# Kernel tuning notes

Hardware: AMD Instinct MI355X
Metric: run time of the kernel (lower is better)

## Reference

```python
import jax, jax.numpy as jnp
import numpy as np

FUSION_RATIO = 0.1


def graph_conv(src, dst, x, W, b, n):
    # DGL GraphConv, norm='both': h = D_in^{-1/2} A D_out^{-1/2} (x W) + b
    ones = jnp.ones((src.shape[0],), x.dtype)
    deg_out = jnp.clip(jax.ops.segment_sum(ones, src, num_segments=n), 1.0)
    deg_in = jnp.clip(jax.ops.segment_sum(ones, dst, num_segments=n), 1.0)
    h = (x @ W) * (deg_out ** -0.5)[:, None]
    agg = jax.ops.segment_sum(h[src], dst, num_segments=n)  # [n, out]
    return agg * (deg_in ** -0.5)[:, None] + b


def norm_embed(e):
    # z-score (unbiased std, matching torch.std) then min-max
    e = (e - e.mean()) / jnp.std(e, ddof=1)
    return (e - e.min()) / (e.max() - e.min())


def setup_inputs() -> dict:
    key = jax.random.key(0)
    ks = jax.random.split(key, 24)
    n_apig, n_fcg = 50000, 100000
    e_apig, e_fcg = 800000, 1600000
    apig_dim, fcg_dim, hidden, united, ncls = 256, 128, 128, 64, 10
    s = 0.05
    inp = {
        'apig_feat': jax.random.normal(ks[0], (n_apig, apig_dim), jnp.float32),
        'fcg_feat': jax.random.normal(ks[1], (n_fcg, fcg_dim), jnp.float32),
        'W_a1': jax.random.normal(ks[2], (apig_dim, hidden), jnp.float32) * s,
        'b_a1': jnp.zeros((hidden,), jnp.float32),
        'W_a2': jax.random.normal(ks[3], (hidden, hidden), jnp.float32) * s,
        'b_a2': jnp.zeros((hidden,), jnp.float32),
        'W_f1': jax.random.normal(ks[4], (fcg_dim, hidden), jnp.float32) * s,
        'b_f1': jnp.zeros((hidden,), jnp.float32),
        'W_f2': jax.random.normal(ks[5], (hidden, hidden), jnp.float32) * s,
        'b_f2': jnp.zeros((hidden,), jnp.float32),
        'W1': jax.random.normal(ks[6], (hidden, united), jnp.float32) * s,
        'b1': jnp.zeros((united,), jnp.float32),
        'W2': jax.random.normal(ks[7], (united, hidden), jnp.float32) * s,
        'b2': jnp.zeros((hidden,), jnp.float32),
        'W_attn': jax.random.normal(ks[8], (hidden, 1), jnp.float32) * s,
        'b_attn': jnp.zeros((1,), jnp.float32),
        'W_cls': jax.random.normal(ks[9], (hidden, ncls), jnp.float32) * s,
        'b_cls': jnp.zeros((ncls,), jnp.float32),
        'apig_src': jax.random.randint(ks[10], (e_apig,), 0, n_apig, jnp.int32),
        'apig_dst': jax.random.randint(ks[11], (e_apig,), 0, n_apig, jnp.int32),
        'fcg_src': jax.random.randint(ks[12], (e_fcg,), 0, n_fcg, jnp.int32),
        'fcg_dst': jax.random.randint(ks[13], (e_fcg,), 0, n_fcg, jnp.int32),
        'n_apig': n_apig,
        'n_fcg': n_fcg,
    }
    return inp


def reference(apig_feat, fcg_feat, W_a1, b_a1, W_a2, b_a2, W_f1, b_f1, W_f2, b_f2,
              W1, b1, W2, b2, W_attn, b_attn, W_cls, b_cls,
              apig_src, apig_dst, fcg_src, fcg_dst, n_apig, n_fcg):
    h_a1 = jax.nn.relu(graph_conv(apig_src, apig_dst, apig_feat, W_a1, b_a1, n_apig))
    h_f1 = jax.nn.relu(graph_conv(fcg_src, fcg_dst, fcg_feat, W_f1, b_f1, n_fcg))
    a_enc = h_a1 @ W1 + b1
    f_enc = h_f1 @ W1 + b1
    a_sum = a_enc.sum(axis=0)
    f_sum = f_enc.sum(axis=0)
    a_enc = a_enc + FUSION_RATIO * f_sum
    f_enc = f_enc + FUSION_RATIO * a_sum
    a_dec = a_enc @ W2 + b2
    f_dec = f_enc @ W2 + b2
    h_a2 = jax.nn.relu(graph_conv(apig_src, apig_dst, a_dec, W_a2, b_a2, n_apig))
    h_f2 = jax.nn.relu(graph_conv(fcg_src, fcg_dst, f_dec, W_f2, b_f2, n_fcg))
    apig_emb = h_a2.mean(axis=0)  # dgl.mean_nodes, single graph -> [hidden]
    fcg_emb = h_f2.max(axis=0)    # dgl.max_nodes -> [hidden]
    a = norm_embed(apig_emb)
    f = norm_embed(fcg_emb)
    wa = jax.nn.softmax(a @ W_attn + b_attn, axis=0)  # [1] -> 1.0
    wf = jax.nn.softmax(f @ W_attn + b_attn, axis=0)
    emb = a * wa + f * wf
    # dropout is identity at inference
    return emb @ W_cls + b_cls
```

## Files before the change

### kernel.cpp

```cpp
#include <hip/hip_runtime.h>
#include <math.h>


typedef __attribute__((ext_vector_type(8))) short bf16x8;
typedef __attribute__((ext_vector_type(8))) unsigned short u16x8;
typedef __attribute__((ext_vector_type(4))) float f32x4;

#define SORT_T 4096

static __device__ inline unsigned short f2bf(float f) {
  unsigned u = __float_as_uint(f);
  unsigned r = (u + 0x7fff + ((u >> 16) & 1)) >> 16;
  return (unsigned short)r;
}
static __device__ inline float bf2f(unsigned short h) {
  return __uint_as_float(((unsigned)h) << 16);
}

__global__ void zero_small_kernel(float* __restrict__ s0, float* __restrict__ s1, int ns,
                                  float* __restrict__ ea, unsigned* __restrict__ ef, int ne,
                                  int* __restrict__ offs_a, int* __restrict__ offs_src_a,
                                  int n_a, int e_a,
                                  int* __restrict__ offs_f, int* __restrict__ offs_src_f,
                                  int n_f, int e_f) {
  int i = threadIdx.x;
  if (i < ns) { s0[i] = 0.f; s1[i] = 0.f; }
  if (i < ne) { ea[i] = 0.f; ef[i] = 0u; }
  if (i == 0) {
    offs_a[n_a] = e_a;
    offs_src_a[n_a] = e_a;
    offs_f[n_f] = e_f;
    offs_src_f[n_f] = e_f;
  }
}

__global__ __launch_bounds__(256) void prep_bt_kernel(
    const float* __restrict__ W_a1, const float* __restrict__ W_f1,
    const float* __restrict__ W_a2, const float* __restrict__ W_f2,
    const float* __restrict__ W1, const float* __restrict__ W2,
    unsigned short* __restrict__ T_a1, unsigned short* __restrict__ T_f1,
    unsigned short* __restrict__ T_a2, unsigned short* __restrict__ T_f2,
    unsigned short* __restrict__ T1, unsigned short* __restrict__ T2) {
  const float* src;
  unsigned short* dst;
  int K, N;
  switch (blockIdx.y) {
    case 0: src = W_a1; dst = T_a1; K = 256; N = 128; break;
    case 1: src = W_f1; dst = T_f1; K = 128; N = 128; break;
    case 2: src = W_a2; dst = T_a2; K = 128; N = 128; break;
    case 3: src = W_f2; dst = T_f2; K = 128; N = 128; break;
    case 4: src = W1;   dst = T1;   K = 128; N = 64;  break;
    default: src = W2;  dst = T2;   K = 64;  N = 128; break;
  }
  int total = K * N;
  for (int idx = blockIdx.x * 256 + threadIdx.x; idx < total; idx += gridDim.x * 256) {
    int n = idx / K, k = idx - n * K;
    dst[idx] = f2bf(src[(size_t)k * N + n]);
  }
}

static __device__ inline int edge_key(const int* __restrict__ a_key,
                                      const int* __restrict__ f_key, int e_a, int i) {
  return (i < e_a) ? a_key[i] : (f_key[i - e_a] + 65536);
}

__global__ __launch_bounds__(256) void radix_hist_kernel(
    const int* __restrict__ a_key, const int* __restrict__ f_key, int e_a, int E,
    int* __restrict__ blkhist, int B) {
  __shared__ int h[512];
  for (int i = threadIdx.x; i < 512; i += 256) h[i] = 0;
  __syncthreads();
  int base = blockIdx.x * SORT_T;
  int end = base + SORT_T;
  if (end > E) end = E;
  for (int i = base + threadIdx.x; i < end; i += 256)
    atomicAdd(&h[edge_key(a_key, f_key, e_a, i) >> 9], 1);
  __syncthreads();
  for (int i = threadIdx.x; i < 512; i += 256) blkhist[i * B + blockIdx.x] = h[i];
}

__global__ __launch_bounds__(256) void cursor_kernel(int* __restrict__ blkhist, int B,
                                                     int* __restrict__ bintotal) {
  __shared__ int part[256];
  int* row = blkhist + (size_t)blockIdx.x * B;
  int C = (B + 255) / 256;
  int start = threadIdx.x * C;
  int end = start + C;
  if (end > B) end = B;
  int v[8];
  int s = 0;
  for (int j = start; j < end; ++j) {
    v[j - start] = row[j];
    s += v[j - start];
  }
  part[threadIdx.x] = s;
  __syncthreads();
  for (int o = 1; o < 256; o <<= 1) {
    int u = (threadIdx.x >= o) ? part[threadIdx.x - o] : 0;
    __syncthreads();
    part[threadIdx.x] += u;
    __syncthreads();
  }
  int run = part[threadIdx.x] - s;
  for (int j = start; j < end; ++j) {
    row[j] = run;
    run += v[j - start];
  }
  if (threadIdx.x == 255) bintotal[blockIdx.x] = part[255];
}

__global__ __launch_bounds__(256) void binscan_kernel(const int* __restrict__ bintotal,
                                                      int* __restrict__ binstart) {
  __shared__ int x[512];
  x[threadIdx.x] = bintotal[threadIdx.x];
  x[threadIdx.x + 256] = bintotal[threadIdx.x + 256];
  __syncthreads();
  for (int o = 1; o < 512; o <<= 1) {
    int i0 = threadIdx.x, i1 = threadIdx.x + 256;
    int v0 = (i0 >= o) ? x[i0 - o] : 0;
    int v1 = (i1 >= o) ? x[i1 - o] : 0;
    __syncthreads();
    x[i0] += v0;
    x[i1] += v1;
    __syncthreads();
  }
  binstart[threadIdx.x] = x[threadIdx.x] - bintotal[threadIdx.x];
  binstart[threadIdx.x + 256] = x[threadIdx.x + 256] - bintotal[threadIdx.x + 256];
}

__global__ __launch_bounds__(256) void scatter_dst_kernel(
    const int* __restrict__ a_key, const int* __restrict__ f_key,
    const int* __restrict__ a_pay, const int* __restrict__ f_pay,
    int e_a, int E, const int* __restrict__ blkhist, int B,
    const int* __restrict__ binstart, int* __restrict__ opack) {
  __shared__ int cur[512];
  int b = blockIdx.x;
  for (int bin = threadIdx.x; bin < 512; bin += 256)
    cur[bin] = binstart[bin] + blkhist[bin * B + b];
  __syncthreads();
  int base = b * SORT_T;
  int end = base + SORT_T;
  if (end > E) end = E;
  for (int i = base + threadIdx.x; i < end; i += 256) {
    int k = edge_key(a_key, f_key, e_a, i);
    int pay = (i < e_a) ? a_pay[i] : f_pay[i - e_a];
    int pos = atomicAdd(&cur[k >> 9], 1);
    opack[pos] = ((k & 511) << 17) | pay;
  }
}

__global__ __launch_bounds__(256) void scatter_src_kernel(
    const int* __restrict__ a_key, const int* __restrict__ f_key,
    int e_a, int E, const int* __restrict__ blkhist, int B,
    const int* __restrict__ binstart, unsigned short* __restrict__ okey) {
  __shared__ int cur[512];
  int b = blockIdx.x;
  for (int bin = threadIdx.x; bin < 512; bin += 256)
    cur[bin] = binstart[bin] + blkhist[bin * B + b];
  __syncthreads();
  int base = b * SORT_T;
  int end = base + SORT_T;
  if (end > E) end = E;
  for (int i = base + threadIdx.x; i < end; i += 256) {
    int k = edge_key(a_key, f_key, e_a, i);
    int pos = atomicAdd(&cur[k >> 9], 1);
    okey[pos] = (unsigned short)(k & 511);
  }
}

__global__ __launch_bounds__(256) void bucket_dst_kernel(
    const int* __restrict__ kp, const int* __restrict__ binstart, int E, int e_a,
    int* __restrict__ csr, int* __restrict__ offs_a, int n_a,
    int* __restrict__ offs_f, int n_f) {
  __shared__ int h[512], x[512], cur[512];
  int b = blockIdx.x;
  int s = binstart[b];
  int e = (b == 511) ? E : binstart[b + 1];
  for (int i = threadIdx.x; i < 512; i += 256) h[i] = 0;
  __syncthreads();
  for (int i = s + threadIdx.x; i < e; i += 256) atomicAdd(&h[kp[i] >> 17], 1);
  __syncthreads();
  for (int i = threadIdx.x; i < 512; i += 256) x[i] = h[i];
  __syncthreads();
  for (int o = 1; o < 512; o <<= 1) {
    int i0 = threadIdx.x, i1 = threadIdx.x + 256;
    int v0 = (i0 >= o) ? x[i0 - o] : 0;
    int v1 = (i1 >= o) ? x[i1 - o] : 0;
    __syncthreads();
    x[i0] += v0;
    x[i1] += v1;
    __syncthreads();
  }
  for (int low = threadIdx.x; low < 512; low += 256) {
    int gpos = s + x[low] - h[low];
    cur[low] = gpos;
    int key = (b << 9) | low;
    if (key < 65536) {
      if (key < n_a) offs_a[key] = gpos;
    } else {
      int v = key - 65536;
      if (v < n_f) offs_f[v] = gpos - e_a;
    }
  }
  __syncthreads();
  for (int i = s + threadIdx.x; i < e; i += 256) {
    int pv = kp[i];
    int pos = atomicAdd(&cur[pv >> 17], 1);
    csr[pos] = pv & 0x1FFFF;
  }
}

__global__ __launch_bounds__(256) void bucket_src_kernel(
    const unsigned short* __restrict__ kl, const int* __restrict__ binstart, int E, int e_a,
    int* __restrict__ offs_src_a, int n_a, int* __restrict__ offs_src_f, int n_f) {
  __shared__ int h[512], x[512];
  int b = blockIdx.x;
  int s = binstart[b];
  int e = (b == 511) ? E : binstart[b + 1];
  for (int i = threadIdx.x; i < 512; i += 256) h[i] = 0;
  __syncthreads();
  for (int i = s + threadIdx.x; i < e; i += 256) atomicAdd(&h[kl[i]], 1);
  __syncthreads();
  for (int i = threadIdx.x; i < 512; i += 256) x[i] = h[i];
  __syncthreads();
  for (int o = 1; o < 512; o <<= 1) {
    int i0 = threadIdx.x, i1 = threadIdx.x + 256;
    int v0 = (i0 >= o) ? x[i0 - o] : 0;
    int v1 = (i1 >= o) ? x[i1 - o] : 0;
    __syncthreads();
    x[i0] += v0;
    x[i1] += v1;
    __syncthreads();
  }
  for (int low = threadIdx.x; low < 512; low += 256) {
    int gpos = s + x[low] - h[low];
    int key = (b << 9) | low;
    if (key < 65536) {
      if (key < n_a) offs_src_a[key] = gpos;
    } else {
      int v = key - 65536;
      if (v < n_f) offs_src_f[v] = gpos - e_a;
    }
  }
}

__global__ void isr_kernel(const int* __restrict__ offs_a, const int* __restrict__ offs_src_a,
                           float* __restrict__ io_a, float* __restrict__ ii_a, int n_a,
                           const int* __restrict__ offs_f, const int* __restrict__ offs_src_f,
                           float* __restrict__ io_f, float* __restrict__ ii_f, int n_f) {
  int i = blockIdx.x * blockDim.x + threadIdx.x;
  if (i < n_a) {
    int ci = offs_a[i + 1] - offs_a[i];
    int co = offs_src_a[i + 1] - offs_src_a[i];
    ii_a[i] = 1.0f / sqrtf((float)(ci < 1 ? 1 : ci));
    io_a[i] = 1.0f / sqrtf((float)(co < 1 ? 1 : co));
  }
  if (i < n_f) {
    int ci = offs_f[i + 1] - offs_f[i];
    int co = offs_src_f[i + 1] - offs_src_f[i];
    ii_f[i] = 1.0f / sqrtf((float)(ci < 1 ? 1 : ci));
    io_f[i] = 1.0f / sqrtf((float)(co < 1 ? 1 : co));
  }
}

template <int K, int N, int INBF16, int ADDV>
__global__ __launch_bounds__(256) void gemm_bls_kernel(
    const void* __restrict__ A, const unsigned short* __restrict__ Bt,
    unsigned short* __restrict__ C, int M,
    const float* __restrict__ add_vec, float add_scale,
    const float* __restrict__ rowscale, const float* __restrict__ bias) {
  constexpr int KS = (K < 128) ? K : 128;
  constexpr int KP = KS + 8;
  constexpr int NT = N / 16;
  constexpr int KK = K / 32;
  constexpr int KKS = KS / 32;
  constexpr int NSTAGE = K / KS;
  constexpr int CHUNKS = (N * KS / 8) / 256;
  __shared__ __align__(16) unsigned short Bs[N * KP];

  const int tid = threadIdx.x;
  const int lane = tid & 63, w = tid >> 6;
  const int q = lane >> 4, l16 = lane & 15;
  const int m0 = blockIdx.x * 64;
  const int m = m0 + w * 16 + l16;
  const int mload = (m < M) ? m : (M - 1);

  bf16x8 af[KK];
  if constexpr (INBF16) {
    const unsigned short* Ar = (const unsigned short*)A + (size_t)mload * K + q * 8;
#pragma unroll
    for (int kk = 0; kk < KK; ++kk)
      af[kk] = *reinterpret_cast<const bf16x8*>(Ar + kk * 32);
  } else {
    const float* Ar = (const float*)A + (size_t)mload * K + q * 8;
    float4 r0[KK], r1[KK];
#pragma unroll
    for (int kk = 0; kk < KK; ++kk) {
      r0[kk] = *reinterpret_cast<const float4*>(Ar + kk * 32);
      r1[kk] = *reinterpret_cast<const float4*>(Ar + kk * 32 + 4);
    }
#pragma unroll
    for (int kk = 0; kk < KK; ++kk) {
      bf16x8 t;
      t[0] = (short)f2bf(r0[kk].x); t[1] = (short)f2bf(r0[kk].y);
      t[2] = (short)f2bf(r0[kk].z); t[3] = (short)f2bf(r0[kk].w);
      t[4] = (short)f2bf(r1[kk].x); t[5] = (short)f2bf(r1[kk].y);
      t[6] = (short)f2bf(r1[kk].z); t[7] = (short)f2bf(r1[kk].w);
      af[kk] = t;
    }
  }
  if constexpr (ADDV) {
#pragma unroll
    for (int kk = 0; kk < KK; ++kk) {
      float4 av0 = *reinterpret_cast<const float4*>(add_vec + kk * 32 + q * 8);
      float4 av1 = *reinterpret_cast<const float4*>(add_vec + kk * 32 + q * 8 + 4);
      u16x8 u = (u16x8)af[kk];
      bf16x8 t;
      t[0] = (short)f2bf(bf2f(u[0]) + add_scale * av0.x);
      t[1] = (short)f2bf(bf2f(u[1]) + add_scale * av0.y);
      t[2] = (short)f2bf(bf2f(u[2]) + add_scale * av0.z);
      t[3] = (short)f2bf(bf2f(u[3]) + add_scale * av0.w);
      t[4] = (short)f2bf(bf2f(u[4]) + add_scale * av1.x);
      t[5] = (short)f2bf(bf2f(u[5]) + add_scale * av1.y);
      t[6] = (short)f2bf(bf2f(u[6]) + add_scale * av1.z);
      t[7] = (short)f2bf(bf2f(u[7]) + add_scale * av1.w);
      af[kk] = t;
    }
  }

  f32x4 acc[NT] = {};
#pragma unroll
  for (int st = 0; st < NSTAGE; ++st) {
    u16x8 breg[CHUNKS];
#pragma unroll
    for (int c = 0; c < CHUNKS; ++c) {
      int idx = c * 256 + tid;
      int n = idx / (KS / 8), kp = (idx % (KS / 8)) * 8;
      breg[c] = *reinterpret_cast<const u16x8*>(Bt + (size_t)n * K + st * KS + kp);
    }
    if (st) __syncthreads();
#pragma unroll
    for (int c = 0; c < CHUNKS; ++c) {
      int idx = c * 256 + tid;
      int n = idx / (KS / 8), kp = (idx % (KS / 8)) * 8;
      *reinterpret_cast<u16x8*>(&Bs[n * KP + kp]) = breg[c];
    }
    __syncthreads();
#pragma unroll
    for (int kk = 0; kk < KKS; ++kk) {
#pragma unroll
      for (int nt = 0; nt < NT; ++nt) {
        bf16x8 bf =
            *reinterpret_cast<const bf16x8*>(&Bs[(nt * 16 + l16) * KP + kk * 32 + q * 8]);
        acc[nt] =
            __builtin_amdgcn_mfma_f32_16x16x32_bf16(bf, af[st * KKS + kk], acc[nt], 0, 0, 0);
      }
    }
  }

  if (m < M) {
    float rs = rowscale ? rowscale[m] : 1.0f;
#pragma unroll
    for (int nt = 0; nt < NT; ++nt) {
      float4 bv;
      if (bias)
        bv = *reinterpret_cast<const float4*>(bias + nt * 16 + q * 4);
      else
        bv = make_float4(0.f, 0.f, 0.f, 0.f);
      ushort4 st4;
      st4.x = f2bf(fmaf(acc[nt][0], rs, bv.x));
      st4.y = f2bf(fmaf(acc[nt][1], rs, bv.y));
      st4.z = f2bf(fmaf(acc[nt][2], rs, bv.z));
      st4.w = f2bf(fmaf(acc[nt][3], rs, bv.w));
      *reinterpret_cast<ushort4*>(C + (size_t)m * N + nt * 16 + q * 4) = st4;
    }
  }
}

__global__ __launch_bounds__(256) void agg_kernel(
    const unsigned short* __restrict__ XW, const int* __restrict__ offs,
    const int* __restrict__ csr, const float* __restrict__ isr_in,
    const float* __restrict__ bias, void* __restrict__ out, int n, int mode) {
  __shared__ float red[8][128];
  int lane = threadIdx.x & 31;
  int g = threadIdx.x >> 5;
  int node = blockIdx.x * 8 + g;
  float4 o = make_float4(0.f, 0.f, 0.f, 0.f);
  if (node < n) {
    int e0 = offs[node], e1 = offs[node + 1];
    float4 a0 = make_float4(0.f, 0.f, 0.f, 0.f);
    float4 a1 = a0, a2 = a0, a3 = a0;
    int e = e0;
    for (; e + 4 <= e1; e += 4) {
      int s0 = csr[e], s1 = csr[e + 1], s2 = csr[e + 2], s3 = csr[e + 3];
      ushort4 v0 = *reinterpret_cast<const ushort4*>(&XW[(size_t)s0 * 128 + lane * 4]);
      ushort4 v1 = *reinterpret_cast<const ushort4*>(&XW[(size_t)s1 * 128 + lane * 4]);
      ushort4 v2 = *reinterpret_cast<const ushort4*>(&XW[(size_t)s2 * 128 + lane * 4]);
      ushort4 v3 = *reinterpret_cast<const ushort4*>(&XW[(size_t)s3 * 128 + lane * 4]);
      a0.x += bf2f(v0.x); a0.y += bf2f(v0.y); a0.z += bf2f(v0.z); a0.w += bf2f(v0.w);
      a1.x += bf2f(v1.x); a1.y += bf2f(v1.y); a1.z += bf2f(v1.z); a1.w += bf2f(v1.w);
      a2.x += bf2f(v2.x); a2.y += bf2f(v2.y); a2.z += bf2f(v2.z); a2.w += bf2f(v2.w);
      a3.x += bf2f(v3.x); a3.y += bf2f(v3.y); a3.z += bf2f(v3.z); a3.w += bf2f(v3.w);
    }
    for (; e < e1; ++e) {
      int s = csr[e];
      ushort4 v = *reinterpret_cast<const ushort4*>(&XW[(size_t)s * 128 + lane * 4]);
      a0.x += bf2f(v.x); a0.y += bf2f(v.y); a0.z += bf2f(v.z); a0.w += bf2f(v.w);
    }
    float4 acc;
    acc.x = (a0.x + a1.x) + (a2.x + a3.x);
    acc.y = (a0.y + a1.y) + (a2.y + a3.y);
    acc.z = (a0.z + a1.z) + (a2.z + a3.z);
    acc.w = (a0.w + a1.w) + (a2.w + a3.w);
    float sc = isr_in[node];
    float4 b = *reinterpret_cast<const float4*>(&bias[lane * 4]);
    o.x = fmaxf(fmaf(acc.x, sc, b.x), 0.f);
    o.y = fmaxf(fmaf(acc.y, sc, b.y), 0.f);
    o.z = fmaxf(fmaf(acc.z, sc, b.z), 0.f);
    o.w = fmaxf(fmaf(acc.w, sc, b.w), 0.f);
  }
  if (mode == 0) {
    if (node < n) {
      ushort4 st;
      st.x = f2bf(o.x); st.y = f2bf(o.y); st.z = f2bf(o.z); st.w = f2bf(o.w);
      *reinterpret_cast<ushort4*>(&((unsigned short*)out)[(size_t)node * 128 + lane * 4]) = st;
    }
    return;
  }
  red[g][lane * 4 + 0] = o.x;
  red[g][lane * 4 + 1] = o.y;
  red[g][lane * 4 + 2] = o.z;
  red[g][lane * 4 + 3] = o.w;
  __syncthreads();
  if (threadIdx.x < 128) {
    float v = red[0][threadIdx.x];
    if (mode == 1) {
#pragma unroll
      for (int j = 1; j < 8; ++j) v += red[j][threadIdx.x];
    } else {
#pragma unroll
      for (int j = 1; j < 8; ++j) v = fmaxf(v, red[j][threadIdx.x]);
    }
    ((float*)out)[(size_t)blockIdx.x * 128 + threadIdx.x] = v;
  }
}

__global__ __launch_bounds__(256) void colsum_kernel(const void* __restrict__ X,
                                                     float* __restrict__ out, int n, int ncol,
                                                     int xbf16) {
  __shared__ float s[256];
  int col = threadIdx.x % ncol;
  int rpb = 256 / ncol;
  int rb = threadIdx.x / ncol;
  float acc = 0.f;
  for (int r = blockIdx.x * rpb + rb; r < n; r += gridDim.x * rpb) {
    size_t idx = (size_t)r * ncol + col;
    acc += xbf16 ? bf2f(((const unsigned short*)X)[idx]) : ((const float*)X)[idx];
  }
  s[threadIdx.x] = acc;
  __syncthreads();
  if (threadIdx.x < ncol) {
    float v = 0.f;
    for (int i = 0; i < rpb; ++i) v += s[threadIdx.x + i * ncol];
    atomicAdd(&out[col], v);
  }
}

__global__ __launch_bounds__(256) void colmax_kernel(const float* __restrict__ X,
                                                     unsigned* __restrict__ out, int n, int ncol) {
  __shared__ float s[256];
  int col = threadIdx.x % ncol;
  int rpb = 256 / ncol;
  int rb = threadIdx.x / ncol;
  float acc = 0.f;
  for (int r = blockIdx.x * rpb + rb; r < n; r += gridDim.x * rpb)
    acc = fmaxf(acc, X[(size_t)r * ncol + col]);
  s[threadIdx.x] = acc;
  __syncthreads();
  if (threadIdx.x < ncol) {
    float v = s[threadIdx.x];
    for (int i = 1; i < rpb; ++i) v = fmaxf(v, s[threadIdx.x + i * ncol]);
    atomicMax(&out[col], __float_as_uint(v));
  }
}

__global__ __launch_bounds__(128) void final_kernel(
    const float* __restrict__ emb_a_sum, const unsigned* __restrict__ emb_f_bits,
    const float* __restrict__ W_cls, const float* __restrict__ b_cls,
    float* __restrict__ out, float inv_n_apig, int ncls) {
  __shared__ float red[128];
  __shared__ float emb[128];
  int t = threadIdx.x;
  float a = emb_a_sum[t] * inv_n_apig;
  float f = __uint_as_float(emb_f_bits[t]);

  float vals[2] = {a, f};
  float norms[2];
#pragma unroll
  for (int which = 0; which < 2; ++which) {
    float x = vals[which];
    red[t] = x;
    __syncthreads();
    for (int o = 64; o > 0; o >>= 1) {
      if (t < o) red[t] += red[t + o];
      __syncthreads();
    }
    float mean = red[0] / 128.f;
    __syncthreads();
    float d = x - mean;
    red[t] = d * d;
    __syncthreads();
    for (int o = 64; o > 0; o >>= 1) {
      if (t < o) red[t] += red[t + o];
      __syncthreads();
    }
    float stdv = sqrtf(red[0] / 127.f);
    __syncthreads();
    float z = d / stdv;
    red[t] = z;
    __syncthreads();
    for (int o = 64; o > 0; o >>= 1) {
      if (t < o) red[t] = fminf(red[t], red[t + o]);
      __syncthreads();
    }
    float zmin = red[0];
    __syncthreads();
    red[t] = z;
    __syncthreads();
    for (int o = 64; o > 0; o >>= 1) {
      if (t < o) red[t] = fmaxf(red[t], red[t + o]);
      __syncthreads();
    }
    float zmax = red[0];
    __syncthreads();
    norms[which] = (z - zmin) / (zmax - zmin);
// ... 11 lines not shown
extern "C" void kernel_launch(void* const* d_in, const int* in_sizes, int n_in,
                              void* d_out, int out_size, void* d_ws, size_t ws_size,
                              hipStream_t stream) {
  const float* apig_feat = (const float*)d_in[0];
  const float* fcg_feat = (const float*)d_in[1];
  const float* W_a1 = (const float*)d_in[2];
  const float* b_a1 = (const float*)d_in[3];
  const float* W_a2 = (const float*)d_in[4];
  const float* b_a2 = (const float*)d_in[5];
  const float* W_f1 = (const float*)d_in[6];
  const float* b_f1 = (const float*)d_in[7];
  const float* W_f2 = (const float*)d_in[8];
  const float* b_f2 = (const float*)d_in[9];
  const float* W1 = (const float*)d_in[10];
  const float* b1 = (const float*)d_in[11];
  const float* W2 = (const float*)d_in[12];
  const float* b2 = (const float*)d_in[13];
  const float* W_cls = (const float*)d_in[16];
  const float* b_cls = (const float*)d_in[17];
  const int* a_src = (const int*)d_in[18];
  const int* a_dst = (const int*)d_in[19];
  const int* f_src = (const int*)d_in[20];
  const int* f_dst = (const int*)d_in[21];

  const int hidden = in_sizes[3];
  const int united = in_sizes[11];
  const int ncls = in_sizes[17];
  const int apig_dim = in_sizes[2] / hidden;
  const int fcg_dim = in_sizes[6] / hidden;
  const int n_a = in_sizes[0] / apig_dim;
  const int n_f = in_sizes[1] / fcg_dim;
  const int e_a = in_sizes[18];
  const int e_f = in_sizes[20];

  char* w = (char*)d_ws;
  auto alloc = [&](size_t bytes) -> void* {
    void* p = (void*)w;
    w += (bytes + 255) & ~(size_t)255;
    return p;
  };
  const int E_tot = e_a + e_f;
  const int B = (E_tot + SORT_T - 1) / SORT_T;
  const int nblkA = (n_a + 7) / 8, nblkF = (n_f + 7) / 8;

  float* isr_out_a = (float*)alloc((size_t)n_a * 4);
  float* isr_in_a = (float*)alloc((size_t)n_a * 4);
  float* isr_out_f = (float*)alloc((size_t)n_f * 4);
  float* isr_in_f = (float*)alloc((size_t)n_f * 4);
  int* offs_a = (int*)alloc((size_t)(n_a + 1) * 4);
  int* offs_f = (int*)alloc((size_t)(n_f + 1) * 4);
  int* offs_src_a = (int*)alloc((size_t)(n_a + 1) * 4);
  int* offs_src_f = (int*)alloc((size_t)(n_f + 1) * 4);
  int* kp = (int*)alloc((size_t)E_tot * 4);
  int* csr = (int*)alloc((size_t)E_tot * 4);
  int* blkhist = (int*)alloc((size_t)512 * B * 4);
  int* bintotal = (int*)alloc((size_t)512 * 4);
  int* binstart = (int*)alloc((size_t)512 * 4);
  unsigned short* G_a = (unsigned short*)alloc((size_t)n_a * hidden * 2);
  unsigned short* H_a = (unsigned short*)alloc((size_t)n_a * hidden * 2);
  unsigned short* G_f = (unsigned short*)alloc((size_t)n_f * hidden * 2);
  unsigned short* H_f = (unsigned short*)alloc((size_t)n_f * hidden * 2);
  float* P = (float*)alloc((size_t)nblkF * hidden * 4);
  unsigned short* E_a = G_a;
  unsigned short* E_f = G_f;
  float* a_sum = (float*)alloc((size_t)united * 4);
  float* f_sum = (float*)alloc((size_t)united * 4);
  float* emb_a = (float*)alloc((size_t)hidden * 4);
  unsigned* emb_f = (unsigned*)alloc((size_t)hidden * 4);
  unsigned short* T_a1 = (unsigned short*)alloc((size_t)apig_dim * hidden * 2);
  unsigned short* T_f1 = (unsigned short*)alloc((size_t)fcg_dim * hidden * 2);
  unsigned short* T_a2 = (unsigned short*)alloc((size_t)hidden * hidden * 2);
  unsigned short* T_f2 = (unsigned short*)alloc((size_t)hidden * hidden * 2);
  unsigned short* T1 = (unsigned short*)alloc((size_t)hidden * united * 2);
  unsigned short* T2 = (unsigned short*)alloc((size_t)united * hidden * 2);
  int* csr_a = csr;
  int* csr_f = csr + e_a;
  unsigned short* ks = (unsigned short*)kp;
  (void)ws_size;
  (void)n_in;
  (void)out_size;

  dim3 blk(256);

  zero_small_kernel<<<1, 128, 0, stream>>>(a_sum, f_sum, united, emb_a, emb_f, hidden,
                                           offs_a, offs_src_a, n_a, e_a,
                                           offs_f, offs_src_f, n_f, e_f);
  prep_bt_kernel<<<dim3(32, 6), blk, 0, stream>>>(W_a1, W_f1, W_a2, W_f2, W1, W2,
                                                  T_a1, T_f1, T_a2, T_f2, T1, T2);

  radix_hist_kernel<<<B, blk, 0, stream>>>(a_dst, f_dst, e_a, E_tot, blkhist, B);
  cursor_kernel<<<512, blk, 0, stream>>>(blkhist, B, bintotal);
  binscan_kernel<<<1, blk, 0, stream>>>(bintotal, binstart);
  scatter_dst_kernel<<<B, blk, 0, stream>>>(a_dst, f_dst, a_src, f_src, e_a, E_tot,
                                            blkhist, B, binstart, kp);
  bucket_dst_kernel<<<512, blk, 0, stream>>>(kp, binstart, E_tot, e_a,
                                             csr, offs_a, n_a, offs_f, n_f);
  radix_hist_kernel<<<B, blk, 0, stream>>>(a_src, f_src, e_a, E_tot, blkhist, B);
  cursor_kernel<<<512, blk, 0, stream>>>(blkhist, B, bintotal);
  binscan_kernel<<<1, blk, 0, stream>>>(bintotal, binstart);
  scatter_src_kernel<<<B, blk, 0, stream>>>(a_src, f_src, e_a, E_tot, blkhist, B,
                                            binstart, ks);
  bucket_src_kernel<<<512, blk, 0, stream>>>(ks, binstart, E_tot, e_a,
                                             offs_src_a, n_a, offs_src_f, n_f);
  isr_kernel<<<(n_f + 255) / 256, blk, 0, stream>>>(offs_a, offs_src_a, isr_out_a, isr_in_a,
                                                    n_a, offs_f, offs_src_f, isr_out_f,
                                                    isr_in_f, n_f);

  const int ga = (n_a + 63) / 64, gf = (n_f + 63) / 64;

  gemm_bls_kernel<256, 128, 0, 0><<<ga, blk, 0, stream>>>(
      apig_feat, T_a1, G_a, n_a, nullptr, 0.f, isr_out_a, nullptr);
  agg_kernel<<<nblkA, blk, 0, stream>>>(G_a, offs_a, csr_a, isr_in_a, b_a1, H_a, n_a, 0);
  gemm_bls_kernel<128, 64, 1, 0><<<ga, blk, 0, stream>>>(
      H_a, T1, E_a, n_a, nullptr, 0.f, nullptr, b1);
  colsum_kernel<<<256, blk, 0, stream>>>(E_a, a_sum, n_a, united, 1);

  gemm_bls_kernel<128, 128, 0, 0><<<gf, blk, 0, stream>>>(
      fcg_feat, T_f1, G_f, n_f, nullptr, 0.f, isr_out_f, nullptr);
  agg_kernel<<<nblkF, blk, 0, stream>>>(G_f, offs_f, csr_f, isr_in_f, b_f1, H_f, n_f, 0);
  gemm_bls_kernel<128, 64, 1, 0><<<gf, blk, 0, stream>>>(
      H_f, T1, E_f, n_f, nullptr, 0.f, nullptr, b1);
  colsum_kernel<<<256, blk, 0, stream>>>(E_f, f_sum, n_f, united, 1);

  gemm_bls_kernel<64, 128, 1, 1><<<ga, blk, 0, stream>>>(
      E_a, T2, H_a, n_a, f_sum, 0.1f, nullptr, b2);
  gemm_bls_kernel<128, 128, 1, 0><<<ga, blk, 0, stream>>>(
      H_a, T_a2, G_a, n_a, nullptr, 0.f, isr_out_a, nullptr);
  agg_kernel<<<nblkA, blk, 0, stream>>>(G_a, offs_a, csr_a, isr_in_a, b_a2, P, n_a, 1);
  colsum_kernel<<<256, blk, 0, stream>>>(P, emb_a, nblkA, hidden, 0);

  gemm_bls_kernel<64, 128, 1, 1><<<gf, blk, 0, stream>>>(
      E_f, T2, H_f, n_f, a_sum, 0.1f, nullptr, b2);
  gemm_bls_kernel<128, 128, 1, 0><<<gf, blk, 0, stream>>>(
      H_f, T_f2, G_f, n_f, nullptr, 0.f, isr_out_f, nullptr);
  agg_kernel<<<nblkF, blk, 0, stream>>>(G_f, offs_f, csr_f, isr_in_f, b_f2, P, n_f, 2);
  colmax_kernel<<<256, blk, 0, stream>>>(P, emb_f, nblkF, hidden);

  final_kernel<<<1, 128, 0, stream>>>(emb_a, emb_f, W_cls, b_cls, (float*)d_out,
                                      1.0f / (float)n_a, ncls);
}
```

Before: 663.3 us.

## Merge apig and fcg branch kernels and fuse sort passes to cut launches

Combines the apig and fcg graph branches into joint launches (dual GEMM, dual aggregation, combined column reductions), so each stage runs once over both graphs. The dst and src radix-sort passes are merged into shared histogram, cursor, scatter and bucket kernels. The bin scans are folded into the consumer kernels, and zero-init is folded into the weight prep kernel. The goal is fewer kernel launches and better GPU fill from larger grids. The cost is extra redundant scans per block, higher shared memory use, and separate partial buffers for the two branches.

```diff
diff --git a/kernel.cpp b/kernel.cpp
--- a/kernel.cpp
+++ b/kernel.cpp
@@ -17,30 +17,40 @@
   return __uint_as_float(((unsigned)h) << 16);
 }
 
-__global__ void zero_small_kernel(float* __restrict__ s0, float* __restrict__ s1, int ns,
-                                  float* __restrict__ ea, unsigned* __restrict__ ef, int ne,
-                                  int* __restrict__ offs_a, int* __restrict__ offs_src_a,
-                                  int n_a, int e_a,
-                                  int* __restrict__ offs_f, int* __restrict__ offs_src_f,
-                                  int n_f, int e_f) {
-  int i = threadIdx.x;
-  if (i < ns) { s0[i] = 0.f; s1[i] = 0.f; }
-  if (i < ne) { ea[i] = 0.f; ef[i] = 0u; }
-  if (i == 0) {
-    offs_a[n_a] = e_a;
-    offs_src_a[n_a] = e_a;
-    offs_f[n_f] = e_f;
-    offs_src_f[n_f] = e_f;
-  }
-}
-
-__global__ __launch_bounds__(256) void prep_bt_kernel(
+static __device__ inline void scan512(int* x) {
+  for (int o = 1; o < 512; o <<= 1) {
+    int i0 = threadIdx.x, i1 = threadIdx.x + 256;
+    int v0 = (i0 >= o) ? x[i0 - o] : 0;
+    int v1 = (i1 >= o) ? x[i1 - o] : 0;
+    __syncthreads();
+    x[i0] += v0;
+    x[i1] += v1;
+    __syncthreads();
+  }
+}
+
+__global__ __launch_bounds__(256) void prep_init_kernel(
     const float* __restrict__ W_a1, const float* __restrict__ W_f1,
     const float* __restrict__ W_a2, const float* __restrict__ W_f2,
     const float* __restrict__ W1, const float* __restrict__ W2,
     unsigned short* __restrict__ T_a1, unsigned short* __restrict__ T_f1,
     unsigned short* __restrict__ T_a2, unsigned short* __restrict__ T_f2,
-    unsigned short* __restrict__ T1, unsigned short* __restrict__ T2) {
+    unsigned short* __restrict__ T1, unsigned short* __restrict__ T2,
+    float* __restrict__ s0, float* __restrict__ s1, int ns,
+    float* __restrict__ ea, unsigned* __restrict__ ef, int ne,
+    int* __restrict__ offs_a, int* __restrict__ offs_src_a, int n_a, int e_a,
+    int* __restrict__ offs_f, int* __restrict__ offs_src_f, int n_f, int e_f) {
+  if (blockIdx.x == 0 && blockIdx.y == 0) {
+    int i = threadIdx.x;
+    if (i < ns) { s0[i] = 0.f; s1[i] = 0.f; }
+    if (i < ne) { ea[i] = 0.f; ef[i] = 0u; }
+    if (i == 0) {
+      offs_a[n_a] = e_a;
+      offs_src_a[n_a] = e_a;
+      offs_f[n_f] = e_f;
+      offs_src_f[n_f] = e_f;
+    }
+  }
   const float* src;
   unsigned short* dst;
   int K, N;
@@ -59,30 +69,36 @@
   }
 }
 
-static __device__ inline int edge_key(const int* __restrict__ a_key,
-                                      const int* __restrict__ f_key, int e_a, int i) {
-  return (i < e_a) ? a_key[i] : (f_key[i - e_a] + 65536);
-}
-
-__global__ __launch_bounds__(256) void radix_hist_kernel(
-    const int* __restrict__ a_key, const int* __restrict__ f_key, int e_a, int E,
-    int* __restrict__ blkhist, int B) {
-  __shared__ int h[512];
-  for (int i = threadIdx.x; i < 512; i += 256) h[i] = 0;
+__global__ __launch_bounds__(256) void hist2_kernel(
+    const int* __restrict__ a_dst, const int* __restrict__ f_dst,
+    const int* __restrict__ a_src, const int* __restrict__ f_src,
+    int e_a, int E, int* __restrict__ blkhistD, int* __restrict__ blkhistS, int B) {
+  __shared__ int hD[512], hS[512];
+  for (int i = threadIdx.x; i < 512; i += 256) { hD[i] = 0; hS[i] = 0; }
   __syncthreads();
   int base = blockIdx.x * SORT_T;
   int end = base + SORT_T;
   if (end > E) end = E;
-  for (int i = base + threadIdx.x; i < end; i += 256)
-    atomicAdd(&h[edge_key(a_key, f_key, e_a, i) >> 9], 1);
-  __syncthreads();
-  for (int i = threadIdx.x; i < 512; i += 256) blkhist[i * B + blockIdx.x] = h[i];
-}
-
-__global__ __launch_bounds__(256) void cursor_kernel(int* __restrict__ blkhist, int B,
-                                                     int* __restrict__ bintotal) {
+  for (int i = base + threadIdx.x; i < end; i += 256) {
+    int kD = (i < e_a) ? a_dst[i] : (f_dst[i - e_a] + 65536);
+    int kS = (i < e_a) ? a_src[i] : (f_src[i - e_a] + 65536);
+    atomicAdd(&hD[kD >> 9], 1);
+    atomicAdd(&hS[kS >> 9], 1);
+  }
+  __syncthreads();
+  for (int i = threadIdx.x; i < 512; i += 256) {
+    blkhistD[i * B + blockIdx.x] = hD[i];
+    blkhistS[i * B + blockIdx.x] = hS[i];
+  }
+}
+
+__global__ __launch_bounds__(256) void cursor2_kernel(
+    int* __restrict__ blkhistD, int* __restrict__ blkhistS, int B,
+    int* __restrict__ bintotalD, int* __restrict__ bintotalS) {
   __shared__ int part[256];
-  int* row = blkhist + (size_t)blockIdx.x * B;
+  int isD = blockIdx.x < 512;
+  int bin = isD ? blockIdx.x : blockIdx.x - 512;
+  int* row = (isD ? blkhistD : blkhistS) + (size_t)bin * B;
   int C = (B + 255) / 256;
   int start = threadIdx.x * C;
   int end = start + C;
@@ -106,140 +122,102 @@
     row[j] = run;
     run += v[j - start];
   }
-  if (threadIdx.x == 255) bintotal[blockIdx.x] = part[255];
-}
-
-__global__ __launch_bounds__(256) void binscan_kernel(const int* __restrict__ bintotal,
-                                                      int* __restrict__ binstart) {
-  __shared__ int x[512];
-  x[threadIdx.x] = bintotal[threadIdx.x];
-  x[threadIdx.x + 256] = bintotal[threadIdx.x + 256];
-  __syncthreads();
-  for (int o = 1; o < 512; o <<= 1) {
-    int i0 = threadIdx.x, i1 = threadIdx.x + 256;
-    int v0 = (i0 >= o) ? x[i0 - o] : 0;
-    int v1 = (i1 >= o) ? x[i1 - o] : 0;
-    __syncthreads();
-    x[i0] += v0;
-    x[i1] += v1;
-    __syncthreads();
-  }
-  binstart[threadIdx.x] = x[threadIdx.x] - bintotal[threadIdx.x];
-  binstart[threadIdx.x + 256] = x[threadIdx.x + 256] - bintotal[threadIdx.x + 256];
-}
-
-__global__ __launch_bounds__(256) void scatter_dst_kernel(
-    const int* __restrict__ a_key, const int* __restrict__ f_key,
-    const int* __restrict__ a_pay, const int* __restrict__ f_pay,
-    int e_a, int E, const int* __restrict__ blkhist, int B,
-    const int* __restrict__ binstart, int* __restrict__ opack) {
-  __shared__ int cur[512];
-  int b = blockIdx.x;
-  for (int bin = threadIdx.x; bin < 512; bin += 256)
-    cur[bin] = binstart[bin] + blkhist[bin * B + b];
+  if (threadIdx.x == 255) (isD ? bintotalD : bintotalS)[bin] = part[255];
+}
+
+__global__ __launch_bounds__(256) void scatter2_kernel(
+    const int* __restrict__ a_dst, const int* __restrict__ f_dst,
+    const int* __restrict__ a_src, const int* __restrict__ f_src,
+    int e_a, int E, const int* __restrict__ blkhistD, const int* __restrict__ blkhistS,
+    int B, const int* __restrict__ bintotalD, const int* __restrict__ bintotalS,
+    int* __restrict__ opack, unsigned short* __restrict__ okey) {
+  __shared__ int curD[512], curS[512], tmp[512];
+  int b = blockIdx.x, tid = threadIdx.x;
+  tmp[tid] = bintotalD[tid];
+  tmp[tid + 256] = bintotalD[tid + 256];
+  __syncthreads();
+  scan512(tmp);
+  curD[tid] = tmp[tid] - bintotalD[tid] + blkhistD[tid * B + b];
+  curD[tid + 256] = tmp[tid + 256] - bintotalD[tid + 256] + blkhistD[(tid + 256) * B + b];
+  __syncthreads();
+  tmp[tid] = bintotalS[tid];
+  tmp[tid + 256] = bintotalS[tid + 256];
+  __syncthreads();
+  scan512(tmp);
+  curS[tid] = tmp[tid] - bintotalS[tid] + blkhistS[tid * B + b];
+  curS[tid + 256] = tmp[tid + 256] - bintotalS[tid + 256] + blkhistS[(tid + 256) * B + b];
   __syncthreads();
   int base = b * SORT_T;
   int end = base + SORT_T;
   if (end > E) end = E;
-  for (int i = base + threadIdx.x; i < end; i += 256) {
-    int k = edge_key(a_key, f_key, e_a, i);
-    int pay = (i < e_a) ? a_pay[i] : f_pay[i - e_a];
-    int pos = atomicAdd(&cur[k >> 9], 1);
-    opack[pos] = ((k & 511) << 17) | pay;
-  }
-}
-
-__global__ __launch_bounds__(256) void scatter_src_kernel(
-    const int* __restrict__ a_key, const int* __restrict__ f_key,
-    int e_a, int E, const int* __restrict__ blkhist, int B,
-    const int* __restrict__ binstart, unsigned short* __restrict__ okey) {
-  __shared__ int cur[512];
-  int b = blockIdx.x;
-  for (int bin = threadIdx.x; bin < 512; bin += 256)
-    cur[bin] = binstart[bin] + blkhist[bin * B + b];
-  __syncthreads();
-  int base = b * SORT_T;
-  int end = base + SORT_T;
-  if (end > E) end = E;
-  for (int i = base + threadIdx.x; i < end; i += 256) {
-    int k = edge_key(a_key, f_key, e_a, i);
-    int pos = atomicAdd(&cur[k >> 9], 1);
-    okey[pos] = (unsigned short)(k & 511);
-  }
-}
-
-__global__ __launch_bounds__(256) void bucket_dst_kernel(
-    const int* __restrict__ kp, const int* __restrict__ binstart, int E, int e_a,
+  for (int i = base + tid; i < end; i += 256) {
+    int sv = (i < e_a) ? a_src[i] : f_src[i - e_a];
+    int kD = (i < e_a) ? a_dst[i] : (f_dst[i - e_a] + 65536);
+    int kS = (i < e_a) ? sv : (sv + 65536);
+    int posD = atomicAdd(&curD[kD >> 9], 1);
+    opack[posD] = ((kD & 511) << 17) | sv;
+    int posS = atomicAdd(&curS[kS >> 9], 1);
+    okey[posS] = (unsigned short)(kS & 511);
+  }
+}
+
+__global__ __launch_bounds__(256) void bucket2_kernel(
+    const int* __restrict__ kp, const unsigned short* __restrict__ ks,
+    const int* __restrict__ bintotalD, const int* __restrict__ bintotalS,
+    int E, int e_a,
     int* __restrict__ csr, int* __restrict__ offs_a, int n_a,
-    int* __restrict__ offs_f, int n_f) {
-  __shared__ int h[512], x[512], cur[512];
-  int b = blockIdx.x;
-  int s = binstart[b];
-  int e = (b == 511) ? E : binstart[b + 1];
-  for (int i = threadIdx.x; i < 512; i += 256) h[i] = 0;
-  __syncthreads();
-  for (int i = s + threadIdx.x; i < e; i += 256) atomicAdd(&h[kp[i] >> 17], 1);
-  __syncthreads();
-  for (int i = threadIdx.x; i < 512; i += 256) x[i] = h[i];
-  __syncthreads();
-  for (int o = 1; o < 512; o <<= 1) {
-    int i0 = threadIdx.x, i1 = threadIdx.x + 256;
-    int v0 = (i0 >= o) ? x[i0 - o] : 0;
-    int v1 = (i1 >= o) ? x[i1 - o] : 0;
-    __syncthreads();
-    x[i0] += v0;
-    x[i1] += v1;
-    __syncthreads();
-  }
-  for (int low = threadIdx.x; low < 512; low += 256) {
-    int gpos = s + x[low] - h[low];
-    cur[low] = gpos;
+    int* __restrict__ offs_f, int n_f,
+    int* __restrict__ offs_src_a, int* __restrict__ offs_src_f) {
+  __shared__ int sh0[512], sh1[512], sh2[512];
+  int tid = threadIdx.x;
+  int isD = blockIdx.x < 512;
+  int b = isD ? blockIdx.x : blockIdx.x - 512;
+  const int* bt = isD ? bintotalD : bintotalS;
+  sh0[tid] = bt[tid];
+  sh0[tid + 256] = bt[tid + 256];
+  __syncthreads();
+  scan512(sh0);
+  int e = sh0[b];
+  int s = e - bt[b];
+  sh1[tid] = 0;
+  sh1[tid + 256] = 0;
+  __syncthreads();
+  if (isD) {
+    for (int i = s + tid; i < e; i += 256) atomicAdd(&sh1[kp[i] >> 17], 1);
+  } else {
+    for (int i = s + tid; i < e; i += 256) atomicAdd(&sh1[ks[i]], 1);
+  }
+  __syncthreads();
+  sh2[tid] = sh1[tid];
+  sh2[tid + 256] = sh1[tid + 256];
+  __syncthreads();
+  scan512(sh2);
+  for (int low = tid; low < 512; low += 256) {
+    int gpos = s + sh2[low] - sh1[low];
     int key = (b << 9) | low;
-    if (key < 65536) {
-      if (key < n_a) offs_a[key] = gpos;
+    if (isD) {
+      sh0[low] = gpos;
+      if (key < 65536) {
+        if (key < n_a) offs_a[key] = gpos;
+      } else {
+        int v = key - 65536;
+        if (v < n_f) offs_f[v] = gpos - e_a;
+      }
     } else {
-      int v = key - 65536;
-      if (v < n_f) offs_f[v] = gpos - e_a;
-    }
-  }
-  __syncthreads();
-  for (int i = s + threadIdx.x; i < e; i += 256) {
-    int pv = kp[i];
-    int pos = atomicAdd(&cur[pv >> 17], 1);
-    csr[pos] = pv & 0x1FFFF;
-  }
-}
-
-__global__ __launch_bounds__(256) void bucket_src_kernel(
-    const unsigned short* __restrict__ kl, const int* __restrict__ binstart, int E, int e_a,
-    int* __restrict__ offs_src_a, int n_a, int* __restrict__ offs_src_f, int n_f) {
-  __shared__ int h[512], x[512];
-  int b = blockIdx.x;
-  int s = binstart[b];
-  int e = (b == 511) ? E : binstart[b + 1];
-  for (int i = threadIdx.x; i < 512; i += 256) h[i] = 0;
-  __syncthreads();
-  for (int i = s + threadIdx.x; i < e; i += 256) atomicAdd(&h[kl[i]], 1);
-  __syncthreads();
-  for (int i = threadIdx.x; i < 512; i += 256) x[i] = h[i];
-  __syncthreads();
-  for (int o = 1; o < 512; o <<= 1) {
-    int i0 = threadIdx.x, i1 = threadIdx.x + 256;
-    int v0 = (i0 >= o) ? x[i0 - o] : 0;
-    int v1 = (i1 >= o) ? x[i1 - o] : 0;
-    __syncthreads();
-    x[i0] += v0;
-    x[i1] += v1;
-    __syncthreads();
-  }
-  for (int low = threadIdx.x; low < 512; low += 256) {
-    int gpos = s + x[low] - h[low];
-    int key = (b << 9) | low;
-    if (key < 65536) {
-      if (key < n_a) offs_src_a[key] = gpos;
-    } else {
-      int v = key - 65536;
-      if (v < n_f) offs_src_f[v] = gpos - e_a;
+      if (key < 65536) {
+        if (key < n_a) offs_src_a[key] = gpos;
+      } else {
+        int v = key - 65536;
+        if (v < n_f) offs_src_f[v] = gpos - e_a;
+      }
+    }
+  }
+  if (isD) {
+    __syncthreads();
+    for (int i = s + tid; i < e; i += 256) {
+      int pv = kp[i];
+      int pos = atomicAdd(&sh0[pv >> 17], 1);
+      csr[pos] = pv & 0x1FFFF;
     }
   }
 }
@@ -264,11 +242,12 @@
 }
 
 template <int K, int N, int INBF16, int ADDV>
-__global__ __launch_bounds__(256) void gemm_bls_kernel(
+static __device__ inline void gemm_body(
     const void* __restrict__ A, const unsigned short* __restrict__ Bt,
-    unsigned short* __restrict__ C, int M,
+    unsigned short* __restrict__ C, int M, int bid,
     const float* __restrict__ add_vec, float add_scale,
-    const float* __restrict__ rowscale, const float* __restrict__ bias) {
+    const float* __restrict__ rowscale, const float* __restrict__ bias,
+    unsigned short* Bs) {
   constexpr int KS = (K < 128) ? K : 128;
   constexpr int KP = KS + 8;
   constexpr int NT = N / 16;
@@ -276,12 +255,11 @@
   constexpr int KKS = KS / 32;
   constexpr int NSTAGE = K / KS;
   constexpr int CHUNKS = (N * KS / 8) / 256;
-  __shared__ __align__(16) unsigned short Bs[N * KP];
 
   const int tid = threadIdx.x;
   const int lane = tid & 63, w = tid >> 6;
   const int q = lane >> 4, l16 = lane & 15;
-  const int m0 = blockIdx.x * 64;
+  const int m0 = bid * 64;
   const int m = m0 + w * 16 + l16;
   const int mload = (m < M) ? m : (M - 1);
 
@@ -335,15 +313,15 @@
 #pragma unroll
     for (int c = 0; c < CHUNKS; ++c) {
       int idx = c * 256 + tid;
-      int n = idx / (KS / 8), kp = (idx % (KS / 8)) * 8;
-      breg[c] = *reinterpret_cast<const u16x8*>(Bt + (size_t)n * K + st * KS + kp);
+      int n = idx / (KS / 8), kpos = (idx % (KS / 8)) * 8;
+      breg[c] = *reinterpret_cast<const u16x8*>(Bt + (size_t)n * K + st * KS + kpos);
     }
     if (st) __syncthreads();
 #pragma unroll
     for (int c = 0; c < CHUNKS; ++c) {
       int idx = c * 256 + tid;
-      int n = idx / (KS / 8), kp = (idx % (KS / 8)) * 8;
-      *reinterpret_cast<u16x8*>(&Bs[n * KP + kp]) = breg[c];
+      int n = idx / (KS / 8), kpos = (idx % (KS / 8)) * 8;
+      *reinterpret_cast<u16x8*>(&Bs[n * KP + kpos]) = breg[c];
     }
     __syncthreads();
 #pragma unroll
@@ -377,14 +355,62 @@
   }
 }
 
-__global__ __launch_bounds__(256) void agg_kernel(
-    const unsigned short* __restrict__ XW, const int* __restrict__ offs,
-    const int* __restrict__ csr, const float* __restrict__ isr_in,
-    const float* __restrict__ bias, void* __restrict__ out, int n, int mode) {
+template <int K, int N, int INBF16, int ADDV>
+__global__ __launch_bounds__(256) void gemm_bls_kernel(
+    const void* __restrict__ A, const unsigned short* __restrict__ Bt,
+    unsigned short* __restrict__ C, int M,
+    const float* __restrict__ add_vec, float add_scale,
+    const float* __restrict__ rowscale, const float* __restrict__ bias) {
+  constexpr int KS = (K < 128) ? K : 128;
+  __shared__ __align__(16) unsigned short Bs[N * (KS + 8)];
+  gemm_body<K, N, INBF16, ADDV>(A, Bt, C, M, blockIdx.x, add_vec, add_scale,
+                                rowscale, bias, Bs);
+}
+
+template <int K, int N, int INBF16, int ADDV>
+__global__ __launch_bounds__(256) void gemm_bls2_kernel(
+    const void* __restrict__ A0, const unsigned short* __restrict__ Bt0,
+    unsigned short* __restrict__ C0, int M0,
+    const void* __restrict__ A1, const unsigned short* __restrict__ Bt1,
+    unsigned short* __restrict__ C1, int M1,
+    const float* __restrict__ av0, const float* __restrict__ av1, float add_scale,
+    const float* __restrict__ rs0, const float* __restrict__ rs1,
+    const float* __restrict__ bias, int gblk) {
+  constexpr int KS = (K < 128) ? K : 128;
+  __shared__ __align__(16) unsigned short Bs[N * (KS + 8)];
+  if ((int)blockIdx.x < gblk) {
+    gemm_body<K, N, INBF16, ADDV>(A0, Bt0, C0, M0, blockIdx.x, av0, add_scale,
+                                  rs0, bias, Bs);
+  } else {
+    gemm_body<K, N, INBF16, ADDV>(A1, Bt1, C1, M1, blockIdx.x - gblk, av1, add_scale,
+                                  rs1, bias, Bs);
+  }
+}
+
+__global__ __launch_bounds__(256) void agg2_kernel(
+    const unsigned short* __restrict__ XW0, const int* __restrict__ offs0,
+    const int* __restrict__ csr0, const float* __restrict__ isr0,
+    const float* __restrict__ bias0, void* __restrict__ out0, int n0, int mode0,
+    const unsigned short* __restrict__ XW1, const int* __restrict__ offs1,
+    const int* __restrict__ csr1, const float* __restrict__ isr1,
+    const float* __restrict__ bias1, void* __restrict__ out1, int n1, int mode1,
+    int nblk0) {
   __shared__ float red[8][128];
+  const unsigned short* XW;
+  const int *offs, *csr;
+  const float *isr_in, *bias;
+  void* out;
+  int n, mode, bid;
+  if ((int)blockIdx.x < nblk0) {
+    XW = XW0; offs = offs0; csr = csr0; isr_in = isr0; bias = bias0;
+    out = out0; n = n0; mode = mode0; bid = blockIdx.x;
+  } else {
+    XW = XW1; offs = offs1; csr = csr1; isr_in = isr1; bias = bias1;
+    out = out1; n = n1; mode = mode1; bid = blockIdx.x - nblk0;
+  }
   int lane = threadIdx.x & 31;
   int g = threadIdx.x >> 5;
-  int node = blockIdx.x * 8 + g;
+  int node = bid * 8 + g;
   float4 o = make_float4(0.f, 0.f, 0.f, 0.f);
   if (node < n) {
     int e0 = offs[node], e1 = offs[node + 1];
@@ -441,22 +467,26 @@
 #pragma unroll
       for (int j = 1; j < 8; ++j) v = fmaxf(v, red[j][threadIdx.x]);
     }
-    ((float*)out)[(size_t)blockIdx.x * 128 + threadIdx.x] = v;
-  }
-}
-
-__global__ __launch_bounds__(256) void colsum_kernel(const void* __restrict__ X,
-                                                     float* __restrict__ out, int n, int ncol,
-                                                     int xbf16) {
+    ((float*)out)[(size_t)bid * 128 + threadIdx.x] = v;
+  }
+}
+
+__global__ __launch_bounds__(256) void colsum2_kernel(
+    const unsigned short* __restrict__ X0, float* __restrict__ out0, int n0,
+    const unsigned short* __restrict__ X1, float* __restrict__ out1, int n1,
+    int ncol) {
   __shared__ float s[256];
+  const unsigned short* X;
+  float* out;
+  int n, bid;
+  if ((int)blockIdx.x < 256) { X = X0; out = out0; n = n0; bid = blockIdx.x; }
+  else { X = X1; out = out1; n = n1; bid = blockIdx.x - 256; }
   int col = threadIdx.x % ncol;
   int rpb = 256 / ncol;
   int rb = threadIdx.x / ncol;
   float acc = 0.f;
-  for (int r = blockIdx.x * rpb + rb; r < n; r += gridDim.x * rpb) {
-    size_t idx = (size_t)r * ncol + col;
-    acc += xbf16 ? bf2f(((const unsigned short*)X)[idx]) : ((const float*)X)[idx];
-  }
+  for (int r = bid * rpb + rb; r < n; r += 256 * rpb)
+    acc += bf2f(X[(size_t)r * ncol + col]);
   s[threadIdx.x] = acc;
   __syncthreads();
   if (threadIdx.x < ncol) {
@@ -466,21 +496,36 @@
   }
 }
 
-__global__ __launch_bounds__(256) void colmax_kernel(const float* __restrict__ X,
-                                                     unsigned* __restrict__ out, int n, int ncol) {
+__global__ __launch_bounds__(256) void colfin_kernel(
+    const float* __restrict__ Pa, float* __restrict__ emb_a, int na,
+    const float* __restrict__ Pf, unsigned* __restrict__ emb_f, int nf, int ncol) {
   __shared__ float s[256];
+  int isSum = blockIdx.x < 256;
+  const float* X = isSum ? Pa : Pf;
+  int n = isSum ? na : nf;
+  int bid = isSum ? blockIdx.x : blockIdx.x - 256;
   int col = threadIdx.x % ncol;
   int rpb = 256 / ncol;
   int rb = threadIdx.x / ncol;
   float acc = 0.f;
-  for (int r = blockIdx.x * rpb + rb; r < n; r += gridDim.x * rpb)
-    acc = fmaxf(acc, X[(size_t)r * ncol + col]);
+  if (isSum) {
+    for (int r = bid * rpb + rb; r < n; r += 256 * rpb) acc += X[(size_t)r * ncol + col];
+  } else {
+    for (int r = bid * rpb + rb; r < n; r += 256 * rpb)
+      acc = fmaxf(acc, X[(size_t)r * ncol + col]);
+  }
   s[threadIdx.x] = acc;
   __syncthreads();
   if (threadIdx.x < ncol) {
-    float v = s[threadIdx.x];
-    for (int i = 1; i < rpb; ++i) v = fmaxf(v, s[threadIdx.x + i * ncol]);
-    atomicMax(&out[col], __float_as_uint(v));
+    if (isSum) {
+      float v = 0.f;
+      for (int i = 0; i < rpb; ++i) v += s[threadIdx.x + i * ncol];
+      atomicAdd(&emb_a[col], v);
+    } else {
+      float v = s[threadIdx.x];
+      for (int i = 1; i < rpb; ++i) v = fmaxf(v, s[threadIdx.x + i * ncol]);
+      atomicMax(&emb_f[col], __float_as_uint(v));
+    }
   }
 }
 
@@ -598,15 +643,18 @@
   int* offs_src_a = (int*)alloc((size_t)(n_a + 1) * 4);
   int* offs_src_f = (int*)alloc((size_t)(n_f + 1) * 4);
   int* kp = (int*)alloc((size_t)E_tot * 4);
+  unsigned short* okey = (unsigned short*)alloc((size_t)E_tot * 2);
   int* csr = (int*)alloc((size_t)E_tot * 4);
-  int* blkhist = (int*)alloc((size_t)512 * B * 4);
-  int* bintotal = (int*)alloc((size_t)512 * 4);
-  int* binstart = (int*)alloc((size_t)512 * 4);
+  int* blkhistD = (int*)alloc((size_t)512 * B * 4);
+  int* blkhistS = (int*)alloc((size_t)512 * B * 4);
+  int* bintotalD = (int*)alloc((size_t)512 * 4);
+  int* bintotalS = (int*)alloc((size_t)512 * 4);
   unsigned short* G_a = (unsigned short*)alloc((size_t)n_a * hidden * 2);
   unsigned short* H_a = (unsigned short*)alloc((size_t)n_a * hidden * 2);
   unsigned short* G_f = (unsigned short*)alloc((size_t)n_f * hidden * 2);
   unsigned short* H_f = (unsigned short*)alloc((size_t)n_f * hidden * 2);
-  float* P = (float*)alloc((size_t)nblkF * hidden * 4);
+  float* P_a = (float*)alloc((size_t)nblkA * hidden * 4);
+  float* P_f = (float*)alloc((size_t)nblkF * hidden * 4);
   unsigned short* E_a = G_a;
   unsigned short* E_f = G_f;
   float* a_sum = (float*)alloc((size_t)united * 4);
@@ -621,33 +669,26 @@
   unsigned short* T2 = (unsigned short*)alloc((size_t)united * hidden * 2);
   int* csr_a = csr;
   int* csr_f = csr + e_a;
-  unsigned short* ks = (unsigned short*)kp;
   (void)ws_size;
   (void)n_in;
   (void)out_size;
 
   dim3 blk(256);
 
-  zero_small_kernel<<<1, 128, 0, stream>>>(a_sum, f_sum, united, emb_a, emb_f, hidden,
-                                           offs_a, offs_src_a, n_a, e_a,
-                                           offs_f, offs_src_f, n_f, e_f);
-  prep_bt_kernel<<<dim3(32, 6), blk, 0, stream>>>(W_a1, W_f1, W_a2, W_f2, W1, W2,
-                                                  T_a1, T_f1, T_a2, T_f2, T1, T2);
-
-  radix_hist_kernel<<<B, blk, 0, stream>>>(a_dst, f_dst, e_a, E_tot, blkhist, B);
-  cursor_kernel<<<512, blk, 0, stream>>>(blkhist, B, bintotal);
-  binscan_kernel<<<1, blk, 0, stream>>>(bintotal, binstart);
-  scatter_dst_kernel<<<B, blk, 0, stream>>>(a_dst, f_dst, a_src, f_src, e_a, E_tot,
-                                            blkhist, B, binstart, kp);
-  bucket_dst_kernel<<<512, blk, 0, stream>>>(kp, binstart, E_tot, e_a,
-                                             csr, offs_a, n_a, offs_f, n_f);
-  radix_hist_kernel<<<B, blk, 0, stream>>>(a_src, f_src, e_a, E_tot, blkhist, B);
-  cursor_kernel<<<512, blk, 0, stream>>>(blkhist, B, bintotal);
-  binscan_kernel<<<1, blk, 0, stream>>>(bintotal, binstart);
-  scatter_src_kernel<<<B, blk, 0, stream>>>(a_src, f_src, e_a, E_tot, blkhist, B,
-                                            binstart, ks);
-  bucket_src_kernel<<<512, blk, 0, stream>>>(ks, binstart, E_tot, e_a,
-                                             offs_src_a, n_a, offs_src_f, n_f);
+  prep_init_kernel<<<dim3(32, 6), blk, 0, stream>>>(
+      W_a1, W_f1, W_a2, W_f2, W1, W2, T_a1, T_f1, T_a2, T_f2, T1, T2,
+      a_sum, f_sum, united, emb_a, emb_f, hidden,
+      offs_a, offs_src_a, n_a, e_a, offs_f, offs_src_f, n_f, e_f);
+
+  hist2_kernel<<<B, blk, 0, stream>>>(a_dst, f_dst, a_src, f_src, e_a, E_tot,
+                                      blkhistD, blkhistS, B);
+  cursor2_kernel<<<1024, blk, 0, stream>>>(blkhistD, blkhistS, B, bintotalD, bintotalS);
+  scatter2_kernel<<<B, blk, 0, stream>>>(a_dst, f_dst, a_src, f_src, e_a, E_tot,
+                                         blkhistD, blkhistS, B, bintotalD, bintotalS,
+                                         kp, okey);
+  bucket2_kernel<<<1024, blk, 0, stream>>>(kp, okey, bintotalD, bintotalS, E_tot, e_a,
+                                           csr, offs_a, n_a, offs_f, n_f,
+                                           offs_src_a, offs_src_f);
   isr_kernel<<<(n_f + 255) / 256, blk, 0, stream>>>(offs_a, offs_src_a, isr_out_a, isr_in_a,
                                                     n_a, offs_f, offs_src_f, isr_out_f,
                                                     isr_in_f, n_f);
@@ -656,32 +697,25 @@
 
   gemm_bls_kernel<256, 128, 0, 0><<<ga, blk, 0, stream>>>(
       apig_feat, T_a1, G_a, n_a, nullptr, 0.f, isr_out_a, nullptr);
-  agg_kernel<<<nblkA, blk, 0, stream>>>(G_a, offs_a, csr_a, isr_in_a, b_a1, H_a, n_a, 0);
-  gemm_bls_kernel<128, 64, 1, 0><<<ga, blk, 0, stream>>>(
-      H_a, T1, E_a, n_a, nullptr, 0.f, nullptr, b1);
-  colsum_kernel<<<256, blk, 0, stream>>>(E_a, a_sum, n_a, united, 1);
-
   gemm_bls_kernel<128, 128, 0, 0><<<gf, blk, 0, stream>>>(
       fcg_feat, T_f1, G_f, n_f, nullptr, 0.f, isr_out_f, nullptr);
-  agg_kernel<<<nblkF, blk, 0, stream>>>(G_f, offs_f, csr_f, isr_in_f, b_f1, H_f, n_f, 0);
-  gemm_bls_kernel<128, 64, 1, 0><<<gf, blk, 0, stream>>>(
-      H_f, T1, E_f, n_f, nullptr, 0.f, nullptr, b1);
-  colsum_kernel<<<256, blk, 0, stream>>>(E_f, f_sum, n_f, united, 1);
-
-  gemm_bls_kernel<64, 128, 1, 1><<<ga, blk, 0, stream>>>(
-      E_a, T2, H_a, n_a, f_sum, 0.1f, nullptr, b2);
-  gemm_bls_kernel<128, 128, 1, 0><<<ga, blk, 0, stream>>>(
-      H_a, T_a2, G_a, n_a, nullptr, 0.f, isr_out_a, nullptr);
-  agg_kernel<<<nblkA, blk, 0, stream>>>(G_a, offs_a, csr_a, isr_in_a, b_a2, P, n_a, 1);
-  colsum_kernel<<<256, blk, 0, stream>>>(P, emb_a, nblkA, hidden, 0);
-
-  gemm_bls_kernel<64, 128, 1, 1><<<gf, blk, 0, stream>>>(
-      E_f, T2, H_f, n_f, a_sum, 0.1f, nullptr, b2);
-  gemm_bls_kernel<128, 128, 1, 0><<<gf, blk, 0, stream>>>(
-      H_f, T_f2, G_f, n_f, nullptr, 0.f, isr_out_f, nullptr);
-  agg_kernel<<<nblkF, blk, 0, stream>>>(G_f, offs_f, csr_f, isr_in_f, b_f2, P, n_f, 2);
-  colmax_kernel<<<256, blk, 0, stream>>>(P, emb_f, nblkF, hidden);
-
+  agg2_kernel<<<nblkA + nblkF, blk, 0, stream>>>(
+      G_a, offs_a, csr_a, isr_in_a, b_a1, H_a, n_a, 0,
+      G_f, offs_f, csr_f, isr_in_f, b_f1, H_f, n_f, 0, nblkA);
+  gemm_bls2_kernel<128, 64, 1, 0><<<ga + gf, blk, 0, stream>>>(
+      H_a, T1, E_a, n_a, H_f, T1, E_f, n_f,
+      nullptr, nullptr, 0.f, nullptr, nullptr, b1, ga);
+  colsum2_kernel<<<512, blk, 0, stream>>>(E_a, a_sum, n_a, E_f, f_sum, n_f, united);
+  gemm_bls2_kernel<64, 128, 1, 1><<<ga + gf, blk, 0, stream>>>(
+      E_a, T2, H_a, n_a, E_f, T2, H_f, n_f,
+      f_sum, a_sum, 0.1f, nullptr, nullptr, b2, ga);
+  gemm_bls2_kernel<128, 128, 1, 0><<<ga + gf, blk, 0, stream>>>(
+      H_a, T_a2, G_a, n_a, H_f, T_f2, G_f, n_f,
+      nullptr, nullptr, 0.f, isr_out_a, isr_out_f, nullptr, ga);
+  agg2_kernel<<<nblkA + nblkF, blk, 0, stream>>>(
+      G_a, offs_a, csr_a, isr_in_a, b_a2, P_a, n_a, 1,
+      G_f, offs_f, csr_f, isr_in_f, b_f2, P_f, n_f, 2, nblkA);
+  colfin_kernel<<<512, blk, 0, stream>>>(P_a, emb_a, nblkA, P_f, emb_f, nblkF, hidden);
   final_kernel<<<1, 128, 0, stream>>>(emb_a, emb_f, W_cls, b_cls, (float*)d_out,
                                       1.0f / (float)n_a, ncls);
 }
```

After: 570.7 us. 1.16x faster.
